# Optimization experiments

Hardware: AMD Instinct MI355X
Metric: run time of the kernel (lower is better)

Reference implementation:

```python
import jax, jax.numpy as jnp
import numpy as np

N_SOTU, N_TAXON, N_EDGES, H = 100000, 50000, 1000000, 128

def setup_inputs() -> dict:
    key = jax.random.key(0)
    ks = jax.random.split(key, 8)
    return {
        "z_sotu": jax.random.normal(ks[0], (N_SOTU, H), dtype=jnp.float32),
        "z_taxon": jax.random.normal(ks[1], (N_TAXON, H), dtype=jnp.float32),
        "row": jax.random.randint(ks[2], (N_EDGES,), 0, N_SOTU, dtype=jnp.int64),
        "col": jax.random.randint(ks[3], (N_EDGES,), 0, N_TAXON, dtype=jnp.int64),
        "w1": jax.random.normal(ks[4], (H, 2 * H), dtype=jnp.float32) * 0.05,
        "b1": jax.random.normal(ks[5], (H,), dtype=jnp.float32) * 0.05,
        "w2": jax.random.normal(ks[6], (1, H), dtype=jnp.float32) * 0.05,
        "b2": jax.random.normal(ks[7], (1,), dtype=jnp.float32) * 0.05,
    }

def reference(z_sotu, z_taxon, row, col, w1, b1, w2, b2):
    # Gather edge endpoints and concat: [E, 2H]
    z = jnp.concatenate([z_sotu[row], z_taxon[col]], axis=-1)
    # 2-layer MLP (torch Linear: y = x @ W.T + b)
    h = jax.nn.relu(jnp.einsum('eh,oh->eo', z, w1) + b1)
    out = jnp.einsum('eh,oh->eo', h, w2) + b2
    return out.reshape(-1)
```

## Files before the change

### kernel.cpp

```cpp
#include <hip/hip_runtime.h>
#include <hip/hip_bf16.h>


#define HID  128
#define FTE  128
#define PST  136

typedef __attribute__((ext_vector_type(8)))  short    bf16x8;
typedef __attribute__((ext_vector_type(16))) float    f32x16;
typedef __attribute__((ext_vector_type(4)))  unsigned uint4v;

__device__ __forceinline__ float bf2f(unsigned short u) {
    return __uint_as_float(((unsigned)u) << 16);
}
__device__ __forceinline__ unsigned pk2(float x, float y) {
    __hip_bfloat162 t = __float22bfloat162_rn(make_float2(x, y));
    return *reinterpret_cast<unsigned*>(&t);
}
__device__ __forceinline__ bf16x8 pack8(float4 a, float4 b) {
    uint4v r;
    r.x = pk2(a.x, a.y); r.y = pk2(a.z, a.w);
    r.z = pk2(b.x, b.y); r.w = pk2(b.z, b.w);
    return *reinterpret_cast<bf16x8*>(&r);
}

__global__ __launch_bounds__(256)
void prep_kernel(const float* __restrict__ zs, const float* __restrict__ zt,
                 const float* __restrict__ w1, const float* __restrict__ b1,
                 unsigned short* __restrict__ U, unsigned short* __restrict__ V,
                 int NS, int NT, int NBU)
{
    __shared__ __align__(16) unsigned short zl[128 * PST];

    const bool isU = (int)blockIdx.x < NBU;
    const float* z      = isU ? zs : zt;
    unsigned short* O   = isU ? U  : V;
    const int N    = isU ? NS : NT;
    const int s0   = (isU ? blockIdx.x : blockIdx.x - NBU) * 128;
    const int koff = isU ? 0 : 128;

    const int tid  = threadIdx.x;
    const int wave = tid >> 6;
    const int lane = tid & 63;
    const int l31  = lane & 31;
    const int hlf  = lane >> 5;

    #pragma unroll
    for (int i = 0; i < 8; ++i) {
        const int f = i * 256 + tid;
        const int r = f >> 4;
        const int c = f & 15;
        int s = s0 + r;
        if (s >= N) s = N - 1;
        const float* src = z + (long long)s * HID + c * 8;
        const float4 a = *(const float4*)(src);
        const float4 b = *(const float4*)(src + 4);
        *(bf16x8*)(zl + r * PST + c * 8) = pack8(a, b);
    }

    bf16x8 afrag[8];
    {
        const float* wrow = w1 + (32 * wave + l31) * 256 + koff + hlf * 8;
        #pragma unroll
        for (int ks = 0; ks < 8; ++ks) {
            const float4 a = *(const float4*)(wrow + ks * 16);
            const float4 b = *(const float4*)(wrow + ks * 16 + 4);
            afrag[ks] = pack8(a, b);
        }
    }
    __syncthreads();

    f32x16 acc[4] = {};
    #pragma unroll
    for (int ks = 0; ks < 8; ++ks) {
        #pragma unroll
        for (int nt = 0; nt < 4; ++nt) {
            const int el = 32 * nt + l31;
            const bf16x8 bfrag = *(const bf16x8*)(zl + el * PST + (2 * ks + hlf) * 8);
            acc[nt] = __builtin_amdgcn_mfma_f32_32x32x16_bf16(afrag[ks], bfrag, acc[nt], 0, 0, 0);
        }
    }

    float b1v[16];
    #pragma unroll
    for (int g = 0; g < 4; ++g) {
        const int hb = 32 * wave + 8 * g + 4 * hlf;
        if (isU) {
            const float4 bb = *(const float4*)(b1 + hb);
            b1v[4*g+0] = bb.x; b1v[4*g+1] = bb.y; b1v[4*g+2] = bb.z; b1v[4*g+3] = bb.w;
        } else {
            b1v[4*g+0] = b1v[4*g+1] = b1v[4*g+2] = b1v[4*g+3] = 0.0f;
        }
    }

    #pragma unroll
    for (int nt = 0; nt < 4; ++nt) {
        const int s = s0 + 32 * nt + l31;
        if (s < N) {
            #pragma unroll
            for (int g = 0; g < 4; ++g) {
                const int cb = 32 * wave + 8 * g + 4 * hlf;
                uint2 o;
                o.x = pk2(acc[nt][4*g+0] + b1v[4*g+0], acc[nt][4*g+1] + b1v[4*g+1]);
                o.y = pk2(acc[nt][4*g+2] + b1v[4*g+2], acc[nt][4*g+3] + b1v[4*g+3]);
                *(uint2*)(O + (long long)s * HID + cb) = o;
            }
        }
    }
}

__global__ __launch_bounds__(256)
void edge_kernel(const unsigned short* __restrict__ U,
                 const unsigned short* __restrict__ V,
                 const int*   __restrict__ row, const int* __restrict__ col,
                 const float* __restrict__ w2, const float* __restrict__ b2,
                 float* __restrict__ out, int E)
{
    const int tid = threadIdx.x;
    const int g   = tid >> 4;
    const int c16 = tid & 15;

    const long long eb = (long long)blockIdx.x * 64 + g * 4;

    int ri[4], ci[4];
    #pragma unroll
    for (int j = 0; j < 4; ++j) {
        long long e = eb + j;
        if (e >= E) e = E - 1;
        ri[j] = row[e]; ci[j] = col[e];
    }
    bf16x8 u[4], v[4];
    #pragma unroll
    for (int j = 0; j < 4; ++j) {
        u[j] = *(const bf16x8*)(U + (long long)ri[j] * HID + c16 * 8);
        v[j] = *(const bf16x8*)(V + (long long)ci[j] * HID + c16 * 8);
    }

    const float4 wa = *(const float4*)(w2 + c16 * 8);
    const float4 wb = *(const float4*)(w2 + c16 * 8 + 4);
    const float w2v[8] = {wa.x, wa.y, wa.z, wa.w, wb.x, wb.y, wb.z, wb.w};

    float p[4] = {0.0f, 0.0f, 0.0f, 0.0f};
    #pragma unroll
    for (int j = 0; j < 4; ++j) {
        #pragma unroll
        for (int k = 0; k < 8; ++k) {
            const float h = fmaxf(bf2f((unsigned short)u[j][k]) +
                                  bf2f((unsigned short)v[j][k]), 0.0f);
            p[j] = fmaf(h, w2v[k], p[j]);
        }
    }
    #pragma unroll
    for (int d = 1; d < 16; d <<= 1) {
        #pragma unroll
        for (int j = 0; j < 4; ++j) p[j] += __shfl_xor(p[j], d, 64);
    }
    if (c16 == 0) {
        const float bb = b2[0];
        if (eb + 3 < E) {
            *(float4*)(out + eb) = make_float4(p[0] + bb, p[1] + bb, p[2] + bb, p[3] + bb);
        } else {
            #pragma unroll
            for (int j = 0; j < 4; ++j)
                if (eb + j < E) out[eb + j] = p[j] + bb;
        }
    }
}

__global__ __launch_bounds__(256, 2)
void edge_mlp_fused(const float* __restrict__ z_sotu, const float* __restrict__ z_taxon,
                    const int* __restrict__ row, const int* __restrict__ col,
                    const float* __restrict__ w1, const float* __restrict__ b1,
                    const float* __restrict__ w2, const float* __restrict__ b2,
                    float* __restrict__ out, int E)
{
    __shared__ __align__(16) unsigned short zsh[FTE * 256];
    const int tid  = threadIdx.x;
    const int wave = tid >> 6;
    const int lane = tid & 63;
    const int l31  = lane & 31;
    const int hlf  = lane >> 5;
    const long long e0 = (long long)blockIdx.x * FTE;
    {
        const int ch  = lane & 15;
        const int rhl = lane >> 4;
        #pragma unroll
        for (int pass = 0; pass < 16; ++pass) {
            const int rh = pass * 4 + rhl;
            const int r  = 32 * wave + (rh >> 1);
            const int hh = rh & 1;
            long long e = e0 + r;
            if (e >= E) e = E - 1;
            const int idx = hh ? col[e] : row[e];
            const float* src = (hh ? z_taxon : z_sotu) + (long long)idx * HID + ch * 8;
            const float4 a = *(const float4*)(src);
            const float4 b = *(const float4*)(src + 4);
            const int c = hh * 16 + ch;
            const int q = c ^ (r & 31);
            *(bf16x8*)(zsh + r * 256 + q * 8) = pack8(a, b);
        }
    }
    bf16x8 afrag[16];
    {
        const float* wrow = w1 + (32 * wave + l31) * 256 + hlf * 8;
        #pragma unroll
        for (int ks = 0; ks < 16; ++ks) {
            const float4 a = *(const float4*)(wrow + ks * 16);
            const float4 b = *(const float4*)(wrow + ks * 16 + 4);
            afrag[ks] = pack8(a, b);
        }
    }
    __syncthreads();
    f32x16 acc[4] = {};
    #pragma unroll
    for (int ks = 0; ks < 16; ++ks) {
        #pragma unroll
        for (int nt = 0; nt < 4; ++nt) {
            const int el = 32 * nt + l31;
            const int q  = (2 * ks + hlf) ^ l31;
            bf16x8 bfrag = *(const bf16x8*)(zsh + el * 256 + q * 8);
            acc[nt] = __builtin_amdgcn_mfma_f32_32x32x16_bf16(afrag[ks], bfrag, acc[nt], 0, 0, 0);
        }
    }
    __syncthreads();
    float* partial = (float*)zsh;
    float b1v[16], w2v[16];
    #pragma unroll
    for (int g = 0; g < 4; ++g) {
        const int hb = 32 * wave + 8 * g + 4 * hlf;
        const float4 bb = *(const float4*)(b1 + hb);
        const float4 ww = *(const float4*)(w2 + hb);
        b1v[4*g+0] = bb.x; b1v[4*g+1] = bb.y; b1v[4*g+2] = bb.z; b1v[4*g+3] = bb.w;
        w2v[4*g+0] = ww.x; w2v[4*g+1] = ww.y; w2v[4*g+2] = ww.z; w2v[4*g+3] = ww.w;
    }
    #pragma unroll
    for (int nt = 0; nt < 4; ++nt) {
        float p = 0.0f;
        #pragma unroll
        for (int r = 0; r < 16; ++r) {
            const float h = fmaxf(acc[nt][r] + b1v[r], 0.0f);
            p = fmaf(h, w2v[r], p);
        }
        p += __shfl_xor(p, 32, 64);
        if (hlf == 0)
            partial[wave * FTE + 32 * nt + l31] = p;
    }
    __syncthreads();
    if (tid < FTE) {
        const long long e = e0 + tid;
        if (e < E) {
            out[e] = partial[0 * FTE + tid] + partial[1 * FTE + tid]
                   + partial[2 * FTE + tid] + partial[3 * FTE + tid]
                   + b2[0];
        }
    }
}

extern "C" void kernel_launch(void* const* d_in, const int* in_sizes, int n_in,
                              void* d_out, int out_size, void* d_ws, size_t ws_size,
                              hipStream_t stream) {
    const float* z_sotu  = (const float*)d_in[0];
    const float* z_taxon = (const float*)d_in[1];
    const int*   row     = (const int*)d_in[2];
    const int*   col     = (const int*)d_in[3];
    const float* w1      = (const float*)d_in[4];
    const float* b1      = (const float*)d_in[5];
    const float* w2      = (const float*)d_in[6];
    const float* b2      = (const float*)d_in[7];
    float*       out     = (float*)d_out;

    const int NS = in_sizes[0] / HID;
    const int NT = in_sizes[1] / HID;
    const int E  = in_sizes[2];
    const size_t need = ((size_t)NS + NT) * HID * 2;

    if (ws_size >= need) {
        unsigned short* U = (unsigned short*)d_ws;
        unsigned short* Vv = U + (size_t)NS * HID;
        const int NBU = (NS + 127) / 128;
        const int NBV = (NT + 127) / 128;
        hipLaunchKernelGGL(prep_kernel, dim3(NBU + NBV), dim3(256), 0, stream,
                           z_sotu, z_taxon, w1, b1, U, Vv, NS, NT, NBU);
        const int nblocks = (E + 63) / 64;
        hipLaunchKernelGGL(edge_kernel, dim3(nblocks), dim3(256), 0, stream,
                           U, Vv, row, col, w2, b2, out, E);
    } else {
        const int nblocks = (E + FTE - 1) / FTE;
        hipLaunchKernelGGL(edge_mlp_fused, dim3(nblocks), dim3(256), 0, stream,
                           z_sotu, z_taxon, row, col, w1, b1, w2, b2, out, E);
    }
}
```

Before: 203.6 us.

## Shrink prep tile to 32 rows and pre-convert W1 to bf16 once

The prep kernel now handles 32 node rows per block instead of 128, which launches four times as many blocks with smaller shared memory and fewer accumulators, to raise occupancy and spread the work across CUs. A new small kernel converts W1 to bf16 once in the workspace, so each block loads ready-made bf16 A fragments instead of converting fp32. The cost is that each block now reloads the W1 fragments while doing a quarter of the MFMA work, plus one extra kernel launch.

```diff
diff --git a/kernel.cpp b/kernel.cpp
--- a/kernel.cpp
+++ b/kernel.cpp
@@ -5,6 +5,7 @@
 #define HID  128
 #define FTE  128
 #define PST  136
+#define PTR  32
 
 typedef __attribute__((ext_vector_type(8)))  short    bf16x8;
 typedef __attribute__((ext_vector_type(16))) float    f32x16;
@@ -25,18 +26,30 @@
 }
 
 __global__ __launch_bounds__(256)
+void w1cvt_kernel(const float* __restrict__ w, unsigned short* __restrict__ ow, int n)
+{
+    const int i = (blockIdx.x * 256 + threadIdx.x) * 8;
+    if (i < n) {
+        const float4 a = *(const float4*)(w + i);
+        const float4 b = *(const float4*)(w + i + 4);
+        *(bf16x8*)(ow + i) = pack8(a, b);
+    }
+}
+
+__global__ __launch_bounds__(256)
 void prep_kernel(const float* __restrict__ zs, const float* __restrict__ zt,
-                 const float* __restrict__ w1, const float* __restrict__ b1,
+                 const unsigned short* __restrict__ w1b,
+                 const float* __restrict__ b1,
                  unsigned short* __restrict__ U, unsigned short* __restrict__ V,
                  int NS, int NT, int NBU)
 {
-    __shared__ __align__(16) unsigned short zl[128 * PST];
+    __shared__ __align__(16) unsigned short zl[PTR * PST];
 
     const bool isU = (int)blockIdx.x < NBU;
     const float* z      = isU ? zs : zt;
     unsigned short* O   = isU ? U  : V;
     const int N    = isU ? NS : NT;
-    const int s0   = (isU ? blockIdx.x : blockIdx.x - NBU) * 128;
+    const int s0   = (isU ? blockIdx.x : blockIdx.x - NBU) * PTR;
     const int koff = isU ? 0 : 128;
 
     const int tid  = threadIdx.x;
@@ -46,7 +59,7 @@
     const int hlf  = lane >> 5;
 
     #pragma unroll
-    for (int i = 0; i < 8; ++i) {
+    for (int i = 0; i < 2; ++i) {
         const int f = i * 256 + tid;
         const int r = f >> 4;
         const int c = f & 15;
@@ -60,25 +73,18 @@
 
     bf16x8 afrag[8];
     {
-        const float* wrow = w1 + (32 * wave + l31) * 256 + koff + hlf * 8;
-        #pragma unroll
-        for (int ks = 0; ks < 8; ++ks) {
-            const float4 a = *(const float4*)(wrow + ks * 16);
-            const float4 b = *(const float4*)(wrow + ks * 16 + 4);
-            afrag[ks] = pack8(a, b);
-        }
-    }
-    __syncthreads();
-
-    f32x16 acc[4] = {};
+        const unsigned short* wrow = w1b + (32 * wave + l31) * 256 + koff + hlf * 8;
+        #pragma unroll
+        for (int ks = 0; ks < 8; ++ks)
+            afrag[ks] = *(const bf16x8*)(wrow + ks * 16);
+    }
+    __syncthreads();
+
+    f32x16 acc = {};
     #pragma unroll
     for (int ks = 0; ks < 8; ++ks) {
-        #pragma unroll
-        for (int nt = 0; nt < 4; ++nt) {
-            const int el = 32 * nt + l31;
-            const bf16x8 bfrag = *(const bf16x8*)(zl + el * PST + (2 * ks + hlf) * 8);
-            acc[nt] = __builtin_amdgcn_mfma_f32_32x32x16_bf16(afrag[ks], bfrag, acc[nt], 0, 0, 0);
-        }
+        const bf16x8 bfrag = *(const bf16x8*)(zl + l31 * PST + (2 * ks + hlf) * 8);
+        acc = __builtin_amdgcn_mfma_f32_32x32x16_bf16(afrag[ks], bfrag, acc, 0, 0, 0);
     }
 
     float b1v[16];
@@ -93,18 +99,15 @@
         }
     }
 
-    #pragma unroll
-    for (int nt = 0; nt < 4; ++nt) {
-        const int s = s0 + 32 * nt + l31;
-        if (s < N) {
-            #pragma unroll
-            for (int g = 0; g < 4; ++g) {
-                const int cb = 32 * wave + 8 * g + 4 * hlf;
-                uint2 o;
-                o.x = pk2(acc[nt][4*g+0] + b1v[4*g+0], acc[nt][4*g+1] + b1v[4*g+1]);
-                o.y = pk2(acc[nt][4*g+2] + b1v[4*g+2], acc[nt][4*g+3] + b1v[4*g+3]);
-                *(uint2*)(O + (long long)s * HID + cb) = o;
-            }
+    const int s = s0 + l31;
+    if (s < N) {
+        #pragma unroll
+        for (int g = 0; g < 4; ++g) {
+            const int cb = 32 * wave + 8 * g + 4 * hlf;
+            uint2 o;
+            o.x = pk2(acc[4*g+0] + b1v[4*g+0], acc[4*g+1] + b1v[4*g+1]);
+            o.y = pk2(acc[4*g+2] + b1v[4*g+2], acc[4*g+3] + b1v[4*g+3]);
+            *(uint2*)(O + (long long)s * HID + cb) = o;
         }
     }
 }
@@ -271,16 +274,20 @@
 
     const int NS = in_sizes[0] / HID;
     const int NT = in_sizes[1] / HID;
+    const int EW = in_sizes[4];
     const int E  = in_sizes[2];
-    const size_t need = ((size_t)NS + NT) * HID * 2;
+    const size_t need = ((size_t)NS + NT) * HID * 2 + (size_t)EW * 2;
 
     if (ws_size >= need) {
-        unsigned short* U = (unsigned short*)d_ws;
-        unsigned short* Vv = U + (size_t)NS * HID;
-        const int NBU = (NS + 127) / 128;
-        const int NBV = (NT + 127) / 128;
+        unsigned short* U   = (unsigned short*)d_ws;
+        unsigned short* Vv  = U + (size_t)NS * HID;
+        unsigned short* w1b = Vv + (size_t)NT * HID;
+        hipLaunchKernelGGL(w1cvt_kernel, dim3((EW / 8 + 255) / 256), dim3(256), 0, stream,
+                           w1, w1b, EW);
+        const int NBU = (NS + PTR - 1) / PTR;
+        const int NBV = (NT + PTR - 1) / PTR;
         hipLaunchKernelGGL(prep_kernel, dim3(NBU + NBV), dim3(256), 0, stream,
-                           z_sotu, z_taxon, w1, b1, U, Vv, NS, NT, NBU);
+                           z_sotu, z_taxon, w1b, b1, U, Vv, NS, NT, NBU);
         const int nblocks = (E + 63) / 64;
         hipLaunchKernelGGL(edge_kernel, dim3(nblocks), dim3(256), 0, stream,
                            U, Vv, row, col, w2, b2, out, E);
```

After: 208.0 us. 2.2% more time.

## Make prep kernel persistent with double-buffered 32-row tiles

Applied to the files above, without the earlier changes.

The prep kernel moves from one block per 128 rows to a fixed grid of 1536 persistent blocks. Each block loops over 32-row tiles and stages the next tile into a second LDS buffer while the MFMAs run on the current one. The W1 fragments are loaded once per block and reused across many tiles, and global loads overlap with compute. In exchange, each tile does fewer MFMAs and a barrier runs every iteration, and the prep kernel is only part of the total time next to the gather-bound edge kernel.

```diff
diff --git a/kernel.cpp b/kernel.cpp
--- a/kernel.cpp
+++ b/kernel.cpp
@@ -5,6 +5,9 @@
 #define HID  128
 #define FTE  128
 #define PST  136
+#define PTR  32
+#define GU   1024
+#define GT   512
 
 typedef __attribute__((ext_vector_type(8)))  short    bf16x8;
 typedef __attribute__((ext_vector_type(16))) float    f32x16;
@@ -28,15 +31,17 @@
 void prep_kernel(const float* __restrict__ zs, const float* __restrict__ zt,
                  const float* __restrict__ w1, const float* __restrict__ b1,
                  unsigned short* __restrict__ U, unsigned short* __restrict__ V,
-                 int NS, int NT, int NBU)
+                 int NS, int NT)
 {
-    __shared__ __align__(16) unsigned short zl[128 * PST];
-
-    const bool isU = (int)blockIdx.x < NBU;
+    __shared__ __align__(16) unsigned short zl[2][PTR * PST];
+
+    const bool isU = (int)blockIdx.x < GU;
     const float* z      = isU ? zs : zt;
     unsigned short* O   = isU ? U  : V;
     const int N    = isU ? NS : NT;
-    const int s0   = (isU ? blockIdx.x : blockIdx.x - NBU) * 128;
+    const int nT   = (N + PTR - 1) / PTR;
+    const int t0   = isU ? blockIdx.x : blockIdx.x - GU;
+    const int step = isU ? GU : GT;
     const int koff = isU ? 0 : 128;
 
     const int tid  = threadIdx.x;
@@ -45,18 +50,24 @@
     const int l31  = lane & 31;
     const int hlf  = lane >> 5;
 
-    #pragma unroll
-    for (int i = 0; i < 8; ++i) {
-        const int f = i * 256 + tid;
-        const int r = f >> 4;
-        const int c = f & 15;
-        int s = s0 + r;
-        if (s >= N) s = N - 1;
-        const float* src = z + (long long)s * HID + c * 8;
-        const float4 a = *(const float4*)(src);
-        const float4 b = *(const float4*)(src + 4);
-        *(bf16x8*)(zl + r * PST + c * 8) = pack8(a, b);
-    }
+    if (t0 >= nT) return;
+
+    auto stage = [&](int t, unsigned short* buf) {
+        #pragma unroll
+        for (int i = 0; i < 2; ++i) {
+            const int f = i * 256 + tid;
+            const int r = f >> 4;
+            const int c = f & 15;
+            int s = t * PTR + r;
+            if (s >= N) s = N - 1;
+            const float* src = z + (long long)s * HID + c * 8;
+            const float4 a = *(const float4*)(src);
+            const float4 b = *(const float4*)(src + 4);
+            *(bf16x8*)(buf + r * PST + c * 8) = pack8(a, b);
+        }
+    };
+
+    stage(t0, zl[0]);
 
     bf16x8 afrag[8];
     {
@@ -68,19 +79,6 @@
             afrag[ks] = pack8(a, b);
         }
     }
-    __syncthreads();
-
-    f32x16 acc[4] = {};
-    #pragma unroll
-    for (int ks = 0; ks < 8; ++ks) {
-        #pragma unroll
-        for (int nt = 0; nt < 4; ++nt) {
-            const int el = 32 * nt + l31;
-            const bf16x8 bfrag = *(const bf16x8*)(zl + el * PST + (2 * ks + hlf) * 8);
-            acc[nt] = __builtin_amdgcn_mfma_f32_32x32x16_bf16(afrag[ks], bfrag, acc[nt], 0, 0, 0);
-        }
-    }
-
     float b1v[16];
     #pragma unroll
     for (int g = 0; g < 4; ++g) {
@@ -92,20 +90,33 @@
             b1v[4*g+0] = b1v[4*g+1] = b1v[4*g+2] = b1v[4*g+3] = 0.0f;
         }
     }
-
-    #pragma unroll
-    for (int nt = 0; nt < 4; ++nt) {
-        const int s = s0 + 32 * nt + l31;
+    __syncthreads();
+
+    int p = 0;
+    for (int t = t0; t < nT; ) {
+        const int tn = t + step;
+        if (tn < nT) stage(tn, zl[p ^ 1]);
+
+        f32x16 acc = {};
+        #pragma unroll
+        for (int ks = 0; ks < 8; ++ks) {
+            const bf16x8 bfrag = *(const bf16x8*)(zl[p] + l31 * PST + (2 * ks + hlf) * 8);
+            acc = __builtin_amdgcn_mfma_f32_32x32x16_bf16(afrag[ks], bfrag, acc, 0, 0, 0);
+        }
+        const int s = t * PTR + l31;
         if (s < N) {
             #pragma unroll
             for (int g = 0; g < 4; ++g) {
                 const int cb = 32 * wave + 8 * g + 4 * hlf;
                 uint2 o;
-                o.x = pk2(acc[nt][4*g+0] + b1v[4*g+0], acc[nt][4*g+1] + b1v[4*g+1]);
-                o.y = pk2(acc[nt][4*g+2] + b1v[4*g+2], acc[nt][4*g+3] + b1v[4*g+3]);
+                o.x = pk2(acc[4*g+0] + b1v[4*g+0], acc[4*g+1] + b1v[4*g+1]);
+                o.y = pk2(acc[4*g+2] + b1v[4*g+2], acc[4*g+3] + b1v[4*g+3]);
                 *(uint2*)(O + (long long)s * HID + cb) = o;
             }
         }
+        __syncthreads();
+        p ^= 1;
+        t = tn;
     }
 }
 
@@ -275,12 +286,10 @@
     const size_t need = ((size_t)NS + NT) * HID * 2;
 
     if (ws_size >= need) {
-        unsigned short* U = (unsigned short*)d_ws;
+        unsigned short* U  = (unsigned short*)d_ws;
         unsigned short* Vv = U + (size_t)NS * HID;
-        const int NBU = (NS + 127) / 128;
-        const int NBV = (NT + 127) / 128;
-        hipLaunchKernelGGL(prep_kernel, dim3(NBU + NBV), dim3(256), 0, stream,
-                           z_sotu, z_taxon, w1, b1, U, Vv, NS, NT, NBU);
+        hipLaunchKernelGGL(prep_kernel, dim3(GU + GT), dim3(256), 0, stream,
+                           z_sotu, z_taxon, w1, b1, U, Vv, NS, NT);
         const int nblocks = (E + 63) / 64;
         hipLaunchKernelGGL(edge_kernel, dim3(nblocks), dim3(256), 0, stream,
                            U, Vv, row, col, w2, b2, out, E);
```

Result: faster. 199.1 us (-2.2%).
